# Kernel optimization log

Hardware: AMD Instinct MI355X
Metric: run time of the kernel (lower is better)

Reference implementation:

```python
import jax, jax.numpy as jnp
import numpy as np

FEAT = 252 * 3  # 756, flattened feature dim


def setup_inputs() -> dict:
    key = jax.random.key(0)
    k1, k2, k3, k4 = jax.random.split(key, 4)
    B, T = 8, 2048
    Q, K, D = 8, 1024, 256  # num_quantizers, codebook_size, embedding_dim
    inputs = jax.random.normal(k1, (B, T, 252, 3), dtype=jnp.float32)
    codebooks = jax.random.normal(k2, (Q, K, D), dtype=jnp.float32) * 0.05
    w_in = jax.random.normal(k3, (FEAT, D), dtype=jnp.float32) * (1.0 / np.sqrt(FEAT))
    w_out = jax.random.normal(k4, (D, FEAT), dtype=jnp.float32) * (1.0 / np.sqrt(D))
    return {"inputs": inputs, "codebooks": codebooks, "w_in": w_in, "w_out": w_out}


def _residual_vq(z, codebooks):
    # z: [B, T, D]; codebooks: [Q, K, D]
    def step(carry, cb):
        residual, quant_sum = carry
        # squared L2 distances: [B, T, K]
        d = (jnp.sum(residual * residual, axis=-1, keepdims=True)
             - 2.0 * jnp.einsum("btd,kd->btk", residual, cb)
             + jnp.sum(cb * cb, axis=-1))
        idx = jnp.argmin(d, axis=-1)          # [B, T]
        q = cb[idx]                            # gather -> [B, T, D]
        return (residual - q, quant_sum + q), (q, idx)

    init = (z, jnp.zeros_like(z))
    (_, quant_sum), (all_q, all_idx) = jax.lax.scan(step, init, codebooks)
    return quant_sum, all_q, all_idx  # [B,T,D], [Q,B,T,D], [Q,B,T]


def reference(inputs, codebooks, w_in, w_out):
    B = inputs.shape[0]
    # (B, T, 252, 3) -> (B, T, 3, 252) -> (B, T, 756)
    x = jnp.transpose(inputs, (0, 1, 3, 2)).reshape(B, -1, FEAT)
    z = jnp.einsum("btf,fd->btd", x, w_in)
    quant_sum, all_q, all_idx = _residual_vq(z, codebooks)
    quantized = jnp.einsum("btd,df->btf", quant_sum, w_out)
    quantized = jax.nn.relu(quantized)
    encoding_indices = jnp.transpose(all_idx, (1, 2, 0))  # [B, T, Q]
    return quantized, all_q, encoding_indices
```

## Files before the change

### kernel.cpp

```cpp
#include <hip/hip_runtime.h>
#include <float.h>

#define M_TOK 16384
#define DIM   256
#define NCODE 1024
#define NQ    8
#define FEAT  756
#define DSCALE 0.00375f
#define LCAP  2560
#define L2CAP 512

using short8 = __attribute__((ext_vector_type(8))) short;
using f32x4  = __attribute__((ext_vector_type(4))) float;

__device__ __forceinline__ float fm(float a, float b) { return __fmul_rn(a, b); }
__device__ __forceinline__ float fa(float a, float b) { return __fadd_rn(a, b); }
__device__ __forceinline__ float fs(float a, float b) { return __fsub_rn(a, b); }

__device__ __forceinline__ unsigned fkey(float f) {
  unsigned b = __float_as_uint(f);
  return (b & 0x80000000u) ? ~b : (b | 0x80000000u);
}
__device__ __forceinline__ float funkey(unsigned k) {
  unsigned b = (k & 0x80000000u) ? (k & 0x7FFFFFFFu) : ~k;
  return __uint_as_float(b);
}
__device__ __forceinline__ unsigned short bf16rne(float x) {
  unsigned b = __float_as_uint(x);
  return (unsigned short)((b + 0x7FFFu + ((b >> 16) & 1u)) >> 16);
}

__device__ float pairwise128_sq(const float* a) {
  float V[8][4];
#pragma unroll
  for (int j = 0; j < 8; ++j)
#pragma unroll
    for (int l = 0; l < 4; ++l) { float x = a[4 * j + l]; V[j][l] = fm(x, x); }
#pragma unroll
  for (int t = 1; t < 4; ++t)
#pragma unroll
    for (int j = 0; j < 8; ++j)
#pragma unroll
      for (int l = 0; l < 4; ++l) {
        float x = a[32 * t + 4 * j + l];
        V[j][l] = fa(V[j][l], fm(x, x));
      }
  float W[4];
#pragma unroll
  for (int l = 0; l < 4; ++l) {
    float p01 = fa(V[0][l], V[1][l]), p23 = fa(V[2][l], V[3][l]);
    float p45 = fa(V[4][l], V[5][l]), p67 = fa(V[6][l], V[7][l]);
    W[l] = fa(fa(p01, p23), fa(p45, p67));
  }
  return fa(fa(W[0], W[2]), fa(W[1], W[3]));
}
__device__ float pairwise256_sq(const float* a) {
  return fa(pairwise128_sq(a), pairwise128_sq(a + 128));
}

__device__ float dot256_np(const float* __restrict__ r, const float* __restrict__ c) {
  float L0 = 0.f, L1 = 0.f, L2 = 0.f, L3 = 0.f;
#pragma unroll 8
  for (int t = 0; t < 64; ++t) {
    float4 rv = *reinterpret_cast<const float4*>(r + 4 * t);
    float4 cv = *reinterpret_cast<const float4*>(c + 4 * t);
    L0 = fa(L0, fm(rv.x, cv.x));
    L1 = fa(L1, fm(rv.y, cv.y));
    L2 = fa(L2, fm(rv.z, cv.z));
    L3 = fa(L3, fm(rv.w, cv.w));
  }
  return fa(fa(L0, L2), fa(L1, L3));
}

__device__ __forceinline__ void np_eval(const float* __restrict__ rrow,
                                        const float* __restrict__ crow,
                                        float t1, float t3, int code,
                                        unsigned long long* __restrict__ dst) {
  float e = dot256_np(rrow, crow);
  float dn = fa(fs(t1, fa(e, e)), t3);
  atomicMin(dst, ((unsigned long long)fkey(dn) << 32) | (unsigned)code);
}

__global__ __launch_bounds__(256) void k_z(const float* __restrict__ in,
                                           const float* __restrict__ w_in,
                                           float* __restrict__ residual) {
  const int m0 = blockIdx.x * 8;
  __shared__ __align__(16) float xp[8][FEAT];
  __shared__ __align__(16) float wsb[2][12][256];
  for (int i = threadIdx.x; i < 8 * FEAT; i += 256) {
    int t = i / FEAT, F = i - t * FEAT;
    int f = F / 3, c = F - f * 3;
    xp[t][c * 252 + f] = in[(size_t)m0 * FEAT + i];
  }
  const int dg = threadIdx.x & 63;
  const int tg = threadIdx.x >> 6;
#pragma unroll
  for (int k = 0; k < 3; ++k) {
    int fi = threadIdx.x + k * 256, row = fi >> 6, col = (fi & 63) * 4;
    *reinterpret_cast<float4*>(&wsb[0][row][col]) =
        *reinterpret_cast<const float4*>(&w_in[(size_t)row * DIM + col]);
  }
  __syncthreads();
  float4 a0 = {0.f, 0.f, 0.f, 0.f}, a1 = {0.f, 0.f, 0.f, 0.f};
  const float* xr0 = &xp[tg * 2 + 0][0];
  const float* xr1 = &xp[tg * 2 + 1][0];
  int cur = 0;
  for (int ch = 0; ch < 63; ++ch) {
    float4 nx[3];
    const bool hn = (ch + 1 < 63);
    if (hn) {
#pragma unroll
      for (int k = 0; k < 3; ++k) {
        int fi = threadIdx.x + k * 256, row = fi >> 6, col = (fi & 63) * 4;
        nx[k] = *reinterpret_cast<const float4*>(
            &w_in[((size_t)(ch + 1) * 12 + row) * DIM + col]);
      }
    }
#pragma unroll
    for (int j4 = 0; j4 < 3; ++j4) {
      float4 x0v = *reinterpret_cast<const float4*>(&xr0[ch * 12 + j4 * 4]);
      float4 x1v = *reinterpret_cast<const float4*>(&xr1[ch * 12 + j4 * 4]);
      float xs0[4] = {x0v.x, x0v.y, x0v.z, x0v.w};
      float xs1[4] = {x1v.x, x1v.y, x1v.z, x1v.w};
#pragma unroll
      for (int jj = 0; jj < 4; ++jj) {
        float4 w4 = *reinterpret_cast<const float4*>(&wsb[cur][j4 * 4 + jj][dg * 4]);
        float x0 = xs0[jj], x1 = xs1[jj];
        a0.x = fa(a0.x, fm(x0, w4.x)); a0.y = fa(a0.y, fm(x0, w4.y));
        a0.z = fa(a0.z, fm(x0, w4.z)); a0.w = fa(a0.w, fm(x0, w4.w));
        a1.x = fa(a1.x, fm(x1, w4.x)); a1.y = fa(a1.y, fm(x1, w4.y));
        a1.z = fa(a1.z, fm(x1, w4.z)); a1.w = fa(a1.w, fm(x1, w4.w));
      }
    }
    if (hn) {
#pragma unroll
      for (int k = 0; k < 3; ++k) {
        int fi = threadIdx.x + k * 256, row = fi >> 6, col = (fi & 63) * 4;
        *reinterpret_cast<float4*>(&wsb[cur ^ 1][row][col]) = nx[k];
      }
    }
    __syncthreads();
    cur ^= 1;
  }
  *reinterpret_cast<float4*>(&residual[(size_t)(m0 + tg * 2 + 0) * DIM + dg * 4]) = a0;
  *reinterpret_cast<float4*>(&residual[(size_t)(m0 + tg * 2 + 1) * DIM + dg * 4]) = a1;
}

__global__ __launch_bounds__(256) void k_cbnorm(const float* __restrict__ cb,
                                                float* __restrict__ cbn) {
  int row = blockIdx.x * 256 + threadIdx.x;
  if (row >= NQ * NCODE) return;
  cbn[row] = pairwise256_sq(&cb[(size_t)row * DIM]);
}

__global__ __launch_bounds__(256) void k_cb16(const float* __restrict__ cb,
                                              unsigned short* __restrict__ cb16) {
  size_t i = (size_t)blockIdx.x * 1024 + (size_t)threadIdx.x * 4;
  float4 v = *reinterpret_cast<const float4*>(&cb[i]);
  ushort4 o;
  o.x = bf16rne(v.x); o.y = bf16rne(v.y); o.z = bf16rne(v.z); o.w = bf16rne(v.w);
  *reinterpret_cast<ushort4*>(&cb16[i]) = o;
}

__global__ __launch_bounds__(256) void k_wt(const float* __restrict__ w_out,
                                            unsigned short* __restrict__ wT16) {
  int n = blockIdx.x, k = threadIdx.x;
  float v = (n < FEAT) ? w_out[(size_t)k * FEAT + n] : 0.f;
  wT16[(size_t)n * DIM + k] = bf16rne(v);
}

__global__ __launch_bounds__(256) void k_t1(const float* __restrict__ residual,
                                            float* __restrict__ t1g,
                                            unsigned long long* __restrict__ best64) {
  int m = blockIdx.x * 256 + threadIdx.x;
  t1g[m] = pairwise256_sq(&residual[(size_t)m * DIM]);
  best64[m] = 0xFFFFFFFFFFFFFFFFull;
}

__global__ __launch_bounds__(512) void k_screen(
    const unsigned short* __restrict__ cb16, const float* __restrict__ cb,
    const float* __restrict__ cbn, float* __restrict__ residual,
    float* __restrict__ t1g, unsigned long long* __restrict__ best64,
    float* __restrict__ allq, float* __restrict__ idxout, int q) {
  __shared__ __align__(16) unsigned short Bs[64][264];
  __shared__ float cbn_s[NCODE];
  __shared__ unsigned list[LCAP];
  __shared__ unsigned list2[L2CAP];
  __shared__ unsigned fbs_u[64];
  __shared__ float t1_s[64], dlt_s[64];
  __shared__ unsigned lcnt, l2cnt;
  const int m0 = blockIdx.x * 64;
  const int tid = threadIdx.x, w = tid >> 6, lane = tid & 63;
  const int lrow = lane & 15, lk = lane >> 4;
  const int wg = w & 3, grp = w >> 2;
  const unsigned short* cbq16 = cb16 + (size_t)q * NCODE * DIM;
  const float* cbqf = cb + (size_t)q * NCODE * DIM;

  for (int i = tid; i < NCODE; i += 512) cbn_s[i] = cbn[q * NCODE + i];
  if (tid < 64) {
    float t1 = t1g[m0 + tid];
    t1_s[tid] = t1;
    dlt_s[tid] = fmaxf(DSCALE * sqrtf(fmaxf(t1, 0.f)), 1e-5f);
    fbs_u[tid] = 0xFFFFFFFFu;
  }
  if (tid == 0) { lcnt = 0; l2cnt = 0; }

  short8 afr[8];
  {
    const float* rrow = &residual[(size_t)(m0 + wg * 16 + lrow) * DIM];
#pragma unroll
    for (int s = 0; s < 8; ++s) {
      float4 x0 = *reinterpret_cast<const float4*>(&rrow[s * 32 + lk * 8]);
      float4 x1 = *reinterpret_cast<const float4*>(&rrow[s * 32 + lk * 8 + 4]);
      short8 t;
      t[0] = (short)bf16rne(x0.x); t[1] = (short)bf16rne(x0.y);
      t[2] = (short)bf16rne(x0.z); t[3] = (short)bf16rne(x0.w);
      t[4] = (short)bf16rne(x1.x); t[5] = (short)bf16rne(x1.y);
      t[6] = (short)bf16rne(x1.z); t[7] = (short)bf16rne(x1.w);
      afr[s] = t;
    }
  }
  __syncthreads();

  const int tokbase = wg * 16 + lk * 4;
  float dl[4];
#pragma unroll
  for (int r = 0; r < 4; ++r) dl[r] = dlt_s[tokbase + r];
  float runmin[4] = {FLT_MAX, FLT_MAX, FLT_MAX, FLT_MAX};
  int runcode[4] = {0, 0, 0, 0};

#define PUSH(PD, PC, R)                                                          \
  {                                                                              \
    unsigned idx_ = atomicAdd(&lcnt, 1u);                                        \
    if (idx_ < LCAP)                                                             \
      list[idx_] = (fkey(PD) & 0xFFFF0000u) |                                    \
                   ((unsigned)(tokbase + (R)) << 10) | (unsigned)(PC);           \
    else                                                                         \
      np_eval(&residual[(size_t)(m0 + tokbase + (R)) * DIM],                     \
              &cbqf[(size_t)(PC) * DIM], t1_s[tokbase + (R)], cbn_s[(PC)],       \
              (PC), &best64[m0 + tokbase + (R)]);                                \
  }

  for (int ct = 0; ct < 16; ++ct) {
    __syncthreads();
    {
#pragma unroll
      for (int k = 0; k < 4; ++k) {
        int f4 = tid + k * 512;
        int row = f4 >> 5, seg = f4 & 31;
        *reinterpret_cast<uint4*>(&Bs[row][seg * 8]) =
            *reinterpret_cast<const uint4*>(&cbq16[(size_t)(ct * 64 + row) * DIM + seg * 8]);
      }
    }
    __syncthreads();

    f32x4 acc[2];
    acc[0] = (f32x4){0.f, 0.f, 0.f, 0.f};
    acc[1] = (f32x4){0.f, 0.f, 0.f, 0.f};
#pragma unroll
    for (int s = 0; s < 8; ++s) {
#pragma unroll
      for (int f2 = 0; f2 < 2; ++f2) {
        const int f = grp * 2 + f2;
        short8 bfr = *reinterpret_cast<const short8*>(&Bs[f * 16 + lrow][s * 32 + lk * 8]);
        acc[f2] = __builtin_amdgcn_mfma_f32_16x16x32_bf16(afr[s], bfr, acc[f2], 0, 0, 0);
      }
    }

#pragma unroll
    for (int f2 = 0; f2 < 2; ++f2) {
      const int code = ct * 64 + (grp * 2 + f2) * 16 + lrow;
      const float t3 = cbn_s[code];
#pragma unroll
      for (int r = 0; r < 4; ++r) {
        const float d = t3 - 2.0f * acc[f2][r];
        if (d < runmin[r]) {
          if (runmin[r] <= d + dl[r]) PUSH(runmin[r], runcode[r], r);
          runmin[r] = d; runcode[r] = code;
        } else if (d <= runmin[r] + dl[r]) {
          PUSH(d, code, r);
        }
      }
    }
  }

  float fb[4] = {runmin[0], runmin[1], runmin[2], runmin[3]};
#pragma unroll
  for (int off = 8; off >= 1; off >>= 1)
#pragma unroll
    for (int r = 0; r < 4; ++r)
      fb[r] = fminf(fb[r], __shfl_xor(fb[r], off, 64));
#pragma unroll
  for (int r = 0; r < 4; ++r)
    if (runmin[r] <= fb[r] + dl[r]) PUSH(runmin[r], runcode[r], r);
  if (lrow == 0)
#pragma unroll
    for (int r = 0; r < 4; ++r)
      atomicMin(&fbs_u[tokbase + r], fkey(fb[r]));
  __syncthreads();

  {
    unsigned n = lcnt; if (n > LCAP) n = LCAP;
    for (unsigned i = tid; i < n; i += 512) {
      unsigned e = list[i];
      unsigned tok = (e >> 10) & 63u;
      float df = funkey(e & 0xFFFF0000u);
      if (df <= funkey(fbs_u[tok]) + dlt_s[tok]) {
        unsigned j = atomicAdd(&l2cnt, 1u);
        if (j < L2CAP) list2[j] = e & 0xFFFFu;
        else np_eval(&residual[(size_t)(m0 + tok) * DIM],
                     &cbqf[(size_t)(e & 1023u) * DIM], t1_s[tok],
                     cbn_s[e & 1023u], (int)(e & 1023u), &best64[m0 + tok]);
      }
    }
  }
  __syncthreads();

  {
    unsigned n2 = l2cnt; if (n2 > L2CAP) n2 = L2CAP;
    const int j4 = lane & 3, g = lane >> 2;
    for (unsigned i0 = (unsigned)w * 16u; i0 < n2; i0 += 128u) {
      unsigned ci = i0 + (unsigned)g;
      bool act = ci < n2;
      unsigned ent = act ? list2[ci] : 0u;
      unsigned tok = (ent >> 10) & 63u, code = ent & 1023u;
      const float* rr = &residual[(size_t)(m0 + tok) * DIM];
      const float* cc2 = &cbqf[(size_t)code * DIM];
      float L = 0.f;
#pragma unroll 8
      for (int t = 0; t < 64; ++t)
        L = fa(L, fm(rr[4 * t + j4], cc2[4 * t + j4]));
      float tmp = fa(L, __shfl_xor(L, 2, 64));
      float e4 = fa(tmp, __shfl_xor(tmp, 1, 64));
      if (act && j4 == 0) {
        float dn = fa(fs(t1_s[tok], fa(e4, e4)), cbn_s[code]);
        atomicMin(&best64[m0 + tok],
                  ((unsigned long long)fkey(dn) << 32) | code);
      }
    }
  }
  __syncthreads();

  for (int t = 0; t < 8; ++t) {
    const int tok = w * 8 + t;
    const size_t m = (size_t)m0 + tok;
    const int ci = (int)(best64[m] & 0xFFFFFFFFull);
    const float4 cv = *reinterpret_cast<const float4*>(&cbqf[(size_t)ci * DIM + lane * 4]);
    const size_t base = m * DIM + lane * 4;
    float4 r = *reinterpret_cast<const float4*>(&residual[base]);
    r.x = fs(r.x, cv.x); r.y = fs(r.y, cv.y); r.z = fs(r.z, cv.z); r.w = fs(r.w, cv.w);
    *reinterpret_cast<float4*>(&residual[base]) = r;
    *reinterpret_cast<float4*>(&allq[((size_t)q * M_TOK + m) * DIM + lane * 4]) = cv;
    float qs[4] = {fm(r.x, r.x), fm(r.y, r.y), fm(r.z, r.z), fm(r.w, r.w)};
    float W[4];
#pragma unroll
    for (int l = 0; l < 4; ++l) {
      float v = qs[l];
      float s1 = __shfl_down(v, 8, 64);
      float s2 = __shfl_down(v, 16, 64);
      float s3 = __shfl_down(v, 24, 64);
      float V = fa(fa(fa(v, s1), s2), s3);
      float A = fa(V, __shfl_down(V, 1, 64));
      float B = fa(A, __shfl_down(A, 2, 64));
      W[l] = fa(B, __shfl_down(B, 4, 64));
    }
    float hsum = fa(fa(W[0], W[2]), fa(W[1], W[3]));
    float up = __shfl(hsum, 32, 64);
    if (lane == 0) {
      t1g[m] = fa(hsum, up);
      best64[m] = 0xFFFFFFFFFFFFFFFFull;
      idxout[m * NQ + q] = (float)ci;
    }
  }
#undef PUSH
}

__global__ __launch_bounds__(256) void k_gemm_out(const float* __restrict__ allq,
                                                  const unsigned short* __restrict__ wT16,
                                                  float* __restrict__ C) {
  __shared__ __align__(16) unsigned short As[64][264];
  __shared__ __align__(16) unsigned short Bs[64][264];
  const int m0 = blockIdx.x * 64;
  const int tid = threadIdx.x, w = tid >> 6, lane = tid & 63;
  const int lrow = lane & 15, lk = lane >> 4;

#pragma unroll
  for (int k4 = 0; k4 < 16; ++k4) {
    int f4 = tid + k4 * 256;
    int tok = f4 >> 6, dseg = f4 & 63;
    float4 v = {0.f, 0.f, 0.f, 0.f};
#pragma unroll
    for (int qq = 0; qq < NQ; ++qq) {
      float4 t = *reinterpret_cast<const float4*>(
          &allq[((size_t)qq * M_TOK + m0 + tok) * DIM + dseg * 4]);
      v.x = fa(v.x, t.x); v.y = fa(v.y, t.y); v.z = fa(v.z, t.z); v.w = fa(v.w, t.w);
    }
    ushort4 o;
    o.x = bf16rne(v.x); o.y = bf16rne(v.y); o.z = bf16rne(v.z); o.w = bf16rne(v.w);
    *reinterpret_cast<ushort4*>(&As[tok][dseg * 4]) = o;
  }
  __syncthreads();

  short8 afr[8];
#pragma unroll
  for (int s = 0; s < 8; ++s)
    afr[s] = *reinterpret_cast<const short8*>(&As[w * 16 + lrow][s * 32 + lk * 8]);

  for (int nt = 0; nt < 12; ++nt) {
    const int n0 = nt * 64;
    __syncthreads();
    {
      int r = tid >> 2, seg = tid & 3;
      const uint4* src = reinterpret_cast<const uint4*>(&wT16[(size_t)(n0 + r) * DIM + seg * 64]);
      uint4* dst = reinterpret_cast<uint4*>(&Bs[r][seg * 64]);
#pragma unroll
      for (int u = 0; u < 8; ++u) dst[u] = src[u];
    }
    __syncthreads();

    f32x4 acc[4];
#pragma unroll
    for (int f = 0; f < 4; ++f) acc[f] = (f32x4){0.f, 0.f, 0.f, 0.f};
#pragma unroll
    for (int s = 0; s < 8; ++s) {
#pragma unroll
      for (int f = 0; f < 4; ++f) {
        short8 bfr = *reinterpret_cast<const short8*>(&Bs[f * 16 + lrow][s * 32 + lk * 8]);
        acc[f] = __builtin_amdgcn_mfma_f32_16x16x32_bf16(afr[s], bfr, acc[f], 0, 0, 0);
      }
    }

#pragma unroll
    for (int f = 0; f < 4; ++f) {
      const int col = n0 + f * 16 + lrow;
      if (col < FEAT) {
#pragma unroll
        for (int r = 0; r < 4; ++r)
          C[(size_t)(m0 + w * 16 + lk * 4 + r) * FEAT + col] = fmaxf(acc[f][r], 0.f);
      }
    }
  }
}

extern "C" void kernel_launch(void* const* d_in, const int* in_sizes, int n_in,
                              void* d_out, int out_size, void* d_ws, size_t ws_size,
                              hipStream_t stream) {
  int i_inputs = 0, i_cb = 1, iA = 2, iB = 3;
  {
    int a = -1, b = -1, ii = -1, ic = -1;
    for (int i = 0; i < n_in; ++i) {
      if (in_sizes[i] == M_TOK * FEAT) ii = i;
      else if (in_sizes[i] == NQ * NCODE * DIM) ic = i;
      else if (in_sizes[i] == FEAT * DIM) { if (a < 0) a = i; else b = i; }
    }
    if (ii >= 0 && ic >= 0 && a >= 0 && b >= 0) { i_inputs = ii; i_cb = ic; iA = a; iB = b; }
  }
  const float* inputs = (const float*)d_in[i_inputs];
  const float* cb     = (const float*)d_in[i_cb];
  const float* w_in   = (const float*)d_in[iA];
  const float* w_out  = (const float*)d_in[iB];

  float* out       = (float*)d_out;
  float* quantized = out;
  float* allq      = out + (size_t)M_TOK * FEAT;
  float* idxout    = allq + (size_t)NQ * M_TOK * DIM;

  float* residual = quantized;

  char* ws = (char*)d_ws;
  unsigned short*     cb16   = (unsigned short*)(ws);
  unsigned short*     wT16   = (unsigned short*)(ws + 4194304);
  float*              cbn    = (float*)(ws + 4587520);
  float*              t1g    = (float*)(ws + 4620288);
  unsigned long long* best64 = (unsigned long long*)(ws + 4685824);

  k_z<<<M_TOK / 8, 256, 0, stream>>>(inputs, w_in, residual);
  k_cbnorm<<<NQ * NCODE / 256, 256, 0, stream>>>(cb, cbn);
  k_cb16<<<NQ * NCODE * DIM / 1024, 256, 0, stream>>>(cb, cb16);
  k_wt<<<768, 256, 0, stream>>>(w_out, wT16);
  k_t1<<<M_TOK / 256, 256, 0, stream>>>(residual, t1g, best64);
  for (int q = 0; q < NQ; ++q)
    k_screen<<<M_TOK / 64, 512, 0, stream>>>(cb16, cb, cbn, residual, t1g, best64,
                                             allq, idxout, q);
  k_gemm_out<<<M_TOK / 64, 256, 0, stream>>>(allq, wT16, quantized);
}
```

Baseline: 665.4 us.

## Double-buffer codebook tiles in k_screen via async global-to-LDS loads with XOR swizzle

```diff
diff --git a/kernel.cpp b/kernel.cpp
--- a/kernel.cpp
+++ b/kernel.cpp
@@ -28,6 +28,12 @@
 __device__ __forceinline__ unsigned short bf16rne(float x) {
   unsigned b = __float_as_uint(x);
   return (unsigned short)((b + 0x7FFFu + ((b >> 16) & 1u)) >> 16);
+}
+
+__device__ __forceinline__ void gload_lds16(const void* g, void* l) {
+  __builtin_amdgcn_global_load_lds(
+      (const __attribute__((address_space(1))) unsigned int*)g,
+      (__attribute__((address_space(3))) unsigned int*)l, 16, 0, 0);
 }
 
 __device__ float pairwise128_sq(const float* a) {
@@ -182,7 +188,7 @@
     const float* __restrict__ cbn, float* __restrict__ residual,
     float* __restrict__ t1g, unsigned long long* __restrict__ best64,
     float* __restrict__ allq, float* __restrict__ idxout, int q) {
-  __shared__ __align__(16) unsigned short Bs[64][264];
+  __shared__ __align__(16) unsigned short BsLin[2 * 64 * 256];
   __shared__ float cbn_s[NCODE];
   __shared__ unsigned list[LCAP];
   __shared__ unsigned list2[L2CAP];
@@ -220,6 +226,21 @@
       afr[s] = t;
     }
   }
+
+#define STAGE(CT, B)                                                             \
+  {                                                                              \
+    _Pragma("unroll")                                                            \
+    for (int k_ = 0; k_ < 4; ++k_) {                                             \
+      int c_ = (w * 4 + k_) * 64 + lane;                            \
+      int row_ = c_ >> 5, c16_ = c_ & 31;                                        \
+      const unsigned short* g_ =                                                 \
+          &cbq16[(size_t)((CT) * 64 + row_) * 256 + (size_t)((c16_ ^ (row_ & 7)) * 8)]; \
+      unsigned short* l_ = &BsLin[(B) * 16384 + (w * 4 + k_) * 512];             \
+      gload_lds16(g_, l_);                                                       \
+    }                                                                            \
+  }
+
+  STAGE(0, 0);
   __syncthreads();
 
   const int tokbase = wg * 16 + lk * 4;
@@ -242,17 +263,8 @@
   }
 
   for (int ct = 0; ct < 16; ++ct) {
-    __syncthreads();
-    {
-#pragma unroll
-      for (int k = 0; k < 4; ++k) {
-        int f4 = tid + k * 512;
-        int row = f4 >> 5, seg = f4 & 31;
-        *reinterpret_cast<uint4*>(&Bs[row][seg * 8]) =
-            *reinterpret_cast<const uint4*>(&cbq16[(size_t)(ct * 64 + row) * DIM + seg * 8]);
-      }
-    }
-    __syncthreads();
+    const int b = ct & 1;
+    if (ct + 1 < 16) STAGE(ct + 1, b ^ 1);
 
     f32x4 acc[2];
     acc[0] = (f32x4){0.f, 0.f, 0.f, 0.f};
@@ -262,7 +274,10 @@
 #pragma unroll
       for (int f2 = 0; f2 < 2; ++f2) {
         const int f = grp * 2 + f2;
-        short8 bfr = *reinterpret_cast<const short8*>(&Bs[f * 16 + lrow][s * 32 + lk * 8]);
+        const int row = f * 16 + lrow;
+        const int chunk = (s * 4 + lk) ^ (lrow & 7);
+        short8 bfr = *reinterpret_cast<const short8*>(
+            &BsLin[b * 16384 + (size_t)row * 256 + chunk * 8]);
         acc[f2] = __builtin_amdgcn_mfma_f32_16x16x32_bf16(afr[s], bfr, acc[f2], 0, 0, 0);
       }
     }
@@ -282,6 +297,7 @@
         }
       }
     }
+    __syncthreads();
   }
 
   float fb[4] = {runmin[0], runmin[1], runmin[2], runmin[3]};
@@ -373,6 +389,7 @@
     }
   }
 #undef PUSH
+#undef STAGE
 }
 
 __global__ __launch_bounds__(256) void k_gemm_out(const float* __restrict__ allq,
```

Result: no change. 655.7 us (-1.5%).
